# Performance work log

Hardware: AMD Instinct MI355X
Metric: run time of the kernel (lower is better)

The kernel has to match this reference:

```python
import jax, jax.numpy as jnp
import numpy as np

WS = 8      # window size
C = 64      # channels
B, H, W = 2, 256, 256
DMAX = 48   # max disparity


def setup_inputs() -> dict:
    key = jax.random.key(0)
    ks = jax.random.split(key, 16)
    n = lambda k, s, sc=1.0: jax.random.normal(k, s, dtype=jnp.float32) * sc
    return {
        'x_left': n(ks[0], (B, C, H, W)),
        'x_right': n(ks[1], (B, C, H, W)),
        'catfea_left': n(ks[2], (B, 4 * C, H, W)),
        'catfea_right': n(ks[3], (B, 4 * C, H, W)),
        'd_left': jax.random.randint(ks[4], (B, H, W), 0, DMAX, dtype=jnp.int32),
        'd_right': jax.random.randint(ks[5], (B, H, W), 0, DMAX, dtype=jnp.int32),
        # BatchNorm2d(4c) affine params (training-mode batch stats used in forward)
        'bn_gamma': jnp.ones((4 * C,), jnp.float32),
        'bn_beta': jnp.zeros((4 * C,), jnp.float32),
        # ResB: two grouped 3x3 convs, groups=4, 4c->4c  => weight [4c, c, 3, 3]
        'rb_w1': n(ks[6], (4 * C, C, 3, 3), 0.05), 'rb_b1': n(ks[7], (4 * C,), 0.05),
        'rb_w2': n(ks[8], (4 * C, C, 3, 3), 0.05), 'rb_b2': n(ks[9], (4 * C,), 0.05),
        # bq/bs: grouped 1x1 convs, groups=4, 4c->c => weight [c, c, 1, 1]
        'bq_w': n(ks[10], (C, C, 1, 1), 0.05), 'bq_b': n(ks[11], (C,), 0.05),
        'bs_w': n(ks[12], (C, C, 1, 1), 0.05), 'bs_b': n(ks[13], (C,), 0.05),
    }


def reference(x_left, x_right, catfea_left, catfea_right, d_left, d_right,
              bn_gamma, bn_beta, rb_w1, rb_b1, rb_w2, rb_b2,
              bq_w, bq_b, bs_w, bs_b):
    b, c, h, w = x_left.shape
    hn, wn = h // WS, w // WS
    P = WS * WS

    def conv(x, wgt, bias, pad):
        y = jax.lax.conv_general_dilated(
            x, wgt, (1, 1), [(pad, pad), (pad, pad)],
            dimension_numbers=('NCHW', 'OIHW', 'NCHW'), feature_group_count=4)
        return y + bias[None, :, None, None]

    def bn(x):
        mu = jnp.mean(x, axis=(0, 2, 3), keepdims=True)
        var = jnp.var(x, axis=(0, 2, 3), keepdims=True)
        return bn_gamma[None, :, None, None] * (x - mu) * jax.lax.rsqrt(var + 1e-5) + bn_beta[None, :, None, None]

    def resb(x):
        y = conv(x, rb_w1, rb_b1, 1)
        y = jnp.where(y > 0, y, 0.1 * y)  # LeakyReLU(0.1)
        y = conv(y, rb_w2, rb_b2, 1)
        return y + x

    # NOTE: faithfully replicates the original reshape-based patchify, which is
    # also applied to [b,h,w,c]-ordered gathered tensors (flat reinterpretation).
    def patchify(t):
        return t.reshape(b, c, hn, WS, wn, WS).transpose(0, 2, 4, 3, 5, 1)

    def unpatchify(t, ch):
        return t.reshape(b, hn, wn, WS, WS, ch).transpose(0, 5, 1, 3, 2, 4).reshape(b, ch, h, w)

    def gather_w(t, idx):  # t:[b,c,h,w], idx:[b,h,w] -> [b,h,w,c]
        return jnp.take_along_axis(t.transpose(0, 2, 3, 1), idx[..., None], axis=2)

    coords_w = jnp.arange(w, dtype=jnp.int32)[None, None, :]
    dl = d_left.astype(jnp.int32)
    dr = d_right.astype(jnp.int32)
    m_left = ((coords_w - dl) >= 0)[:, None].astype(x_left.dtype)
    m_right = ((coords_w + dr) <= w - 1)[:, None].astype(x_right.dtype)
    r2l_w = jnp.maximum(coords_w - dl, 0)
    l2r_w = jnp.minimum(coords_w + dr, w - 1)

    Q = conv(resb(bn(catfea_left)), bq_w, bq_b, 0)
    K = conv(resb(bn(catfea_right)), bs_w, bs_b, 0)

    Q_sel = patchify(gather_w(Q, l2r_w))
    K_sel = patchify(gather_w(K, r2l_w))
    Q_sel = Q_sel - Q_sel.mean((4, 5), keepdims=True)
    K_sel = K_sel - K_sel.mean((4, 5), keepdims=True)

    # per-window [P, c] @ [c, P] batched matmuls
    score_r2l = patchify(Q).reshape(-1, P, c) @ K_sel.transpose(0, 1, 2, 5, 3, 4).reshape(-1, c, P)
    score_l2r = patchify(K).reshape(-1, P, c) @ Q_sel.transpose(0, 1, 2, 5, 3, 4).reshape(-1, c, P)
    Mr2l = jax.nn.softmax(score_r2l, axis=-1)
    Ml2r = jax.nn.softmax(score_l2r, axis=-1)

    def m_relax(M, p=2):  # sum of row-shifted copies (shifts -p..p, zero-padded)
        out = M
        for s in range(1, p + 1):
            out = out + jnp.pad(M[:, :-s, :], ((0, 0), (s, 0), (0, 0)))
            out = out + jnp.pad(M[:, s:, :], ((0, 0), (0, s), (0, 0)))
        return out

    # Valid-mask maps (dead code w.r.t. returned outputs in the original; kept for fidelity)
    V_left = jnp.tanh(5 * unpatchify(jax.lax.stop_gradient(
        jnp.einsum('npq,nqp->np', m_relax(Mr2l), Ml2r)), 1))
    V_right = jnp.tanh(5 * unpatchify(jax.lax.stop_gradient(
        jnp.einsum('npq,nqp->np', m_relax(Ml2r), Mr2l)), 1))
    del V_left, V_right

    x_right_sel = patchify(gather_w(x_right, r2l_w)).reshape(-1, P, c)
    x_left_sel = patchify(gather_w(x_left, l2r_w)).reshape(-1, P, c)
    x_leftT = unpatchify(Mr2l @ x_right_sel, c)
    x_rightT = unpatchify(Ml2r @ x_left_sel, c)

    out_left = x_left + x_leftT * m_left
    out_right = x_right + x_rightT * m_right
    return out_left, out_right
```

## Files before the change

### kernel.cpp

```cpp
#include <hip/hip_runtime.h>


__global__ __launch_bounds__(256) void k_bnstats(
    const float* __restrict__ cat_l, const float* __restrict__ cat_r,
    const float* __restrict__ gamma, const float* __restrict__ beta,
    float* __restrict__ stats)
{
    int ch = blockIdx.x & 255;
    int side = blockIdx.x >> 8;
    const float* src = side ? cat_r : cat_l;
    int tid = threadIdx.x;
    float s = 0.f, s2 = 0.f;
    #pragma unroll
    for (int b = 0; b < 2; ++b) {
        const float* p = src + (size_t)b * 16777216 + (size_t)ch * 65536;
        for (int i = tid; i < 65536; i += 256) {
            float v = p[i];
            s += v; s2 += v * v;
        }
    }
    __shared__ float rs[256], rq[256];
    rs[tid] = s; rq[tid] = s2;
    __syncthreads();
    for (int off = 128; off > 0; off >>= 1) {
        if (tid < off) { rs[tid] += rs[tid + off]; rq[tid] += rq[tid + off]; }
        __syncthreads();
    }
    if (tid == 0) {
        float mean = rs[0] * (1.f / 131072.f);
        float var  = rq[0] * (1.f / 131072.f) - mean * mean;
        float rstd = rsqrtf(var + 1e-5f);
        float sc = gamma[ch] * rstd;
        stats[side * 512 + ch] = sc;
        stats[side * 512 + 256 + ch] = beta[ch] - mean * sc;
    }
}

__global__ __launch_bounds__(256) void k_fold(
    const float* __restrict__ w2, const float* __restrict__ b2,
    const float* __restrict__ bqw, const float* __restrict__ bqb,
    const float* __restrict__ bsw, const float* __restrict__ bsb,
    const float* __restrict__ stats,
    float* __restrict__ WfQ, float* __restrict__ bfQ,
    float* __restrict__ WfK, float* __restrict__ bfK)
{
    int idx = blockIdx.x * 256 + threadIdx.x;
    int j    = idx & 15;
    int ic   = (idx >> 4) & 63;
    int g    = (idx >> 10) & 3;
    int side = (idx >> 12) & 1;
    const float* pw  = side ? bsw : bqw;
    const float* st  = stats + side * 512;
    const float* pwr = pw + (size_t)(g * 16 + j) * 64;
    const float* wbase = w2 + (size_t)(g * 64) * 576 + ic * 9;
    float a[9] = {0.f,0.f,0.f,0.f,0.f,0.f,0.f,0.f,0.f};
    #pragma unroll 4
    for (int oc = 0; oc < 64; ++oc) {
        float p = pwr[oc];
        const float* wrow = wbase + (size_t)oc * 576;
        #pragma unroll
        for (int k = 0; k < 9; ++k) a[k] = fmaf(p, wrow[k], a[k]);
    }
    float* dst = (side ? WfK : WfQ) + (size_t)((g * 64 + ic) * 16 + j) * 12;
    #pragma unroll
    for (int k = 0; k < 9; ++k) dst[k] = a[k];
    dst[9]  = pwr[ic] * st[g * 64 + ic];
    dst[10] = 0.f; dst[11] = 0.f;
    if (ic == 0) {
        float s = (side ? bsb : bqb)[g * 16 + j];
        for (int oc = 0; oc < 64; ++oc)
            s = fmaf(pwr[oc], b2[g * 64 + oc] + st[256 + g * 64 + oc], s);
        (side ? bfK : bfQ)[g * 16 + j] = s;
    }
}

__global__ __launch_bounds__(256) void k_conv1(
    const float* __restrict__ cat, const float* __restrict__ stats,
    const float* __restrict__ w1, const float* __restrict__ b1,
    float* __restrict__ y1)
{
    int blk = blockIdx.x;
    int wt = blk & 7;   blk >>= 3;
    int ht = blk & 7;   blk >>= 3;
    int oh = blk & 3;   blk >>= 2;
    int g  = blk & 3;   blk >>= 2;
    int b  = blk;
    int tid = threadIdx.x;
    int tw = tid & 31, th = tid >> 5;
    int rb = th * 4;
    int h = ht * 32 + rb, w = wt * 32 + tw;

    __shared__ __align__(16) float tile[2][34][36];
    __shared__ __align__(16) float wb[2][16][12];

    float accA[16], accB[16], accC[16], accD[16];
    #pragma unroll
    for (int j = 0; j < 16; ++j) {
        float bb = b1[g * 64 + oh * 16 + j];
        accA[j] = bb; accB[j] = bb; accC[j] = bb; accD[j] = bb;
    }

    const float* catg = cat + ((size_t)b * 256 + g * 64) * 65536;
    const float* wg = w1 + (size_t)(g * 64 + oh * 16) * 576;
    int h0 = ht * 32 - 1, w0 = wt * 32 - 1;

    int soff[5]; int slds[5]; bool sin[5];
    #pragma unroll
    for (int s = 0; s < 5; ++s) {
        int idx = tid + 256 * s;
        int r = idx / 34, c = idx - r * 34;
        bool v = idx < 1156;
        int hh = h0 + r, ww = w0 + c;
        sin[s]  = v && (unsigned)hh < 256u && (unsigned)ww < 256u;
        soff[s] = hh * 256 + ww;
        slds[s] = v ? (r * 36 + c) : (33 * 36 + 35);
    }
    bool wvld = tid < 144;
    int woc = tid / 9, wk = tid - woc * 9;
    const float* wptr = wg + (size_t)woc * 576 + wk;
    int wlds = woc * 12 + wk;

    float t[5], wv, csn, shn;
    float* tile0 = &tile[0][0][0];
    float* wb0 = &wb[0][0][0];

    {
        csn = stats[g * 64]; shn = stats[256 + g * 64];
        #pragma unroll
        for (int s = 0; s < 5; ++s) {
            t[s] = sin[s] ? catg[soff[s]] : 0.f;
            tile0[slds[s]] = sin[s] ? fmaf(t[s], csn, shn) : 0.f;
        }
        if (wvld) wb0[wlds] = wptr[0];
    }
    __syncthreads();

    int cur = 0;
    for (int ic = 0; ic < 64; ++ic) {
        bool pf = (ic + 1 < 64);
        if (pf) {
            const float* plane = catg + (size_t)(ic + 1) * 65536;
            csn = stats[g * 64 + ic + 1];
            shn = stats[256 + g * 64 + ic + 1];
            #pragma unroll
            for (int s = 0; s < 5; ++s) t[s] = sin[s] ? plane[soff[s]] : 0.f;
            wv = wvld ? wptr[(ic + 1) * 9] : 0.f;
        }
        float xr[6][3];
        #pragma unroll
        for (int rr = 0; rr < 6; ++rr)
            #pragma unroll
            for (int cc = 0; cc < 3; ++cc)
                xr[rr][cc] = tile[cur][rb + rr][tw + cc];
        #pragma unroll
        for (int j = 0; j < 16; ++j) {
            float4 wa = *(const float4*)&wb[cur][j][0];
            float4 wc = *(const float4*)&wb[cur][j][4];
            float w8  = wb[cur][j][8];
            float s0 = accA[j], s1 = accB[j], s2 = accC[j], s3 = accD[j];
            s0 = fmaf(wa.x, xr[0][0], s0); s1 = fmaf(wa.x, xr[1][0], s1);
            s2 = fmaf(wa.x, xr[2][0], s2); s3 = fmaf(wa.x, xr[3][0], s3);
            s0 = fmaf(wa.y, xr[0][1], s0); s1 = fmaf(wa.y, xr[1][1], s1);
            s2 = fmaf(wa.y, xr[2][1], s2); s3 = fmaf(wa.y, xr[3][1], s3);
            s0 = fmaf(wa.z, xr[0][2], s0); s1 = fmaf(wa.z, xr[1][2], s1);
            s2 = fmaf(wa.z, xr[2][2], s2); s3 = fmaf(wa.z, xr[3][2], s3);
            s0 = fmaf(wa.w, xr[1][0], s0); s1 = fmaf(wa.w, xr[2][0], s1);
            s2 = fmaf(wa.w, xr[3][0], s2); s3 = fmaf(wa.w, xr[4][0], s3);
            s0 = fmaf(wc.x, xr[1][1], s0); s1 = fmaf(wc.x, xr[2][1], s1);
            s2 = fmaf(wc.x, xr[3][1], s2); s3 = fmaf(wc.x, xr[4][1], s3);
            s0 = fmaf(wc.y, xr[1][2], s0); s1 = fmaf(wc.y, xr[2][2], s1);
            s2 = fmaf(wc.y, xr[3][2], s2); s3 = fmaf(wc.y, xr[4][2], s3);
            s0 = fmaf(wc.z, xr[2][0], s0); s1 = fmaf(wc.z, xr[3][0], s1);
            s2 = fmaf(wc.z, xr[4][0], s2); s3 = fmaf(wc.z, xr[5][0], s3);
            s0 = fmaf(wc.w, xr[2][1], s0); s1 = fmaf(wc.w, xr[3][1], s1);
            s2 = fmaf(wc.w, xr[4][1], s2); s3 = fmaf(wc.w, xr[5][1], s3);
            s0 = fmaf(w8,   xr[2][2], s0); s1 = fmaf(w8,   xr[3][2], s1);
            s2 = fmaf(w8,   xr[4][2], s2); s3 = fmaf(w8,   xr[5][2], s3);
            accA[j] = s0; accB[j] = s1; accC[j] = s2; accD[j] = s3;
        }
        if (pf) {
            float* tn = &tile[cur ^ 1][0][0];
            #pragma unroll
            for (int s = 0; s < 5; ++s)
                tn[slds[s]] = sin[s] ? fmaf(t[s], csn, shn) : 0.f;
            if (wvld) (&wb[cur ^ 1][0][0])[wlds] = wv;
        }
        __syncthreads();
        cur ^= 1;
    }

    float* yp = y1 + ((size_t)b * 256 + g * 64 + oh * 16) * 65536
                   + (size_t)h * 256 + w;
    #pragma unroll
    for (int j = 0; j < 16; ++j) {
        float v0 = accA[j], v1 = accB[j], v2 = accC[j], v3 = accD[j];
        yp[(size_t)j * 65536 +   0] = v0 > 0.f ? v0 : 0.1f * v0;
        yp[(size_t)j * 65536 + 256] = v1 > 0.f ? v1 : 0.1f * v1;
        yp[(size_t)j * 65536 + 512] = v2 > 0.f ? v2 : 0.1f * v2;
        yp[(size_t)j * 65536 + 768] = v3 > 0.f ? v3 : 0.1f * v3;
    }
}

__global__ __launch_bounds__(256) void k_conv2f(
    const float* __restrict__ y1, const float* __restrict__ cat,
    const float* __restrict__ Wf, const float* __restrict__ bf,
    float* __restrict__ Qout)
{
    int blk = blockIdx.x;
    int wt = blk & 7;   blk >>= 3;
    int ht = blk & 7;   blk >>= 3;
    int g  = blk & 3;   blk >>= 2;
    int b  = blk;
    int tid = threadIdx.x;
    int tw = tid & 31, th = tid >> 5;
    int rb = th * 4;
    int h = ht * 32 + rb, w = wt * 32 + tw;

    __shared__ __align__(16) float tile[2][34][36];
    __shared__ __align__(16) float wb[2][16][12];

    float accA[16], accB[16], accC[16], accD[16];
    #pragma unroll
    for (int j = 0; j < 16; ++j) {
        float bb = bf[g * 16 + j];
        accA[j] = bb; accB[j] = bb; accC[j] = bb; accD[j] = bb;
    }

    const float* yg = y1 + ((size_t)b * 256 + g * 64) * 65536;
    const float* catp = cat + ((size_t)b * 256 + g * 64) * 65536
                            + (size_t)h * 256 + w;
    const float* wfg = Wf + (size_t)(g * 64) * 192;
    int h0 = ht * 32 - 1, w0 = wt * 32 - 1;

    int soff[5]; int slds[5]; bool sin[5];
    #pragma unroll
    for (int s = 0; s < 5; ++s) {
        int idx = tid + 256 * s;
        int r = idx / 34, c = idx - r * 34;
        bool v = idx < 1156;
        int hh = h0 + r, ww = w0 + c;
        sin[s]  = v && (unsigned)hh < 256u && (unsigned)ww < 256u;
        soff[s] = hh * 256 + ww;
        slds[s] = v ? (r * 36 + c) : (33 * 36 + 35);
    }
    bool wvld = tid < 192;
    float t[5], wv, cv0, cv1, cv2, cv3, ncv0, ncv1, ncv2, ncv3;
    float* tile0 = &tile[0][0][0];

    {
        #pragma unroll
        for (int s = 0; s < 5; ++s) {
            t[s] = sin[s] ? yg[soff[s]] : 0.f;
            tile0[slds[s]] = t[s];
        }
        if (wvld) (&wb[0][0][0])[tid] = wfg[tid];
        cv0 = catp[0]; cv1 = catp[256]; cv2 = catp[512]; cv3 = catp[768];
    }
    __syncthreads();

    int cur = 0;
    for (int ic = 0; ic < 64; ++ic) {
        bool pf = (ic + 1 < 64);
        if (pf) {
            const float* plane = yg + (size_t)(ic + 1) * 65536;
            #pragma unroll
            for (int s = 0; s < 5; ++s) t[s] = sin[s] ? plane[soff[s]] : 0.f;
            wv = wvld ? wfg[(size_t)(ic + 1) * 192 + tid] : 0.f;
            const float* cp = catp + (size_t)(ic + 1) * 65536;
            ncv0 = cp[0]; ncv1 = cp[256]; ncv2 = cp[512]; ncv3 = cp[768];
        }
        float xr[6][3];
        #pragma unroll
        for (int rr = 0; rr < 6; ++rr)
            #pragma unroll
            for (int cc = 0; cc < 3; ++cc)
                xr[rr][cc] = tile[cur][rb + rr][tw + cc];
        #pragma unroll
        for (int j = 0; j < 16; ++j) {
            float4 wa = *(const float4*)&wb[cur][j][0];
            float4 wc = *(const float4*)&wb[cur][j][4];
            float4 wd = *(const float4*)&wb[cur][j][8];
            float s0 = accA[j], s1 = accB[j], s2 = accC[j], s3 = accD[j];
            s0 = fmaf(wa.x, xr[0][0], s0); s1 = fmaf(wa.x, xr[1][0], s1);
            s2 = fmaf(wa.x, xr[2][0], s2); s3 = fmaf(wa.x, xr[3][0], s3);
            s0 = fmaf(wa.y, xr[0][1], s0); s1 = fmaf(wa.y, xr[1][1], s1);
            s2 = fmaf(wa.y, xr[2][1], s2); s3 = fmaf(wa.y, xr[3][1], s3);
            s0 = fmaf(wa.z, xr[0][2], s0); s1 = fmaf(wa.z, xr[1][2], s1);
            s2 = fmaf(wa.z, xr[2][2], s2); s3 = fmaf(wa.z, xr[3][2], s3);
            s0 = fmaf(wa.w, xr[1][0], s0); s1 = fmaf(wa.w, xr[2][0], s1);
            s2 = fmaf(wa.w, xr[3][0], s2); s3 = fmaf(wa.w, xr[4][0], s3);
            s0 = fmaf(wc.x, xr[1][1], s0); s1 = fmaf(wc.x, xr[2][1], s1);
            s2 = fmaf(wc.x, xr[3][1], s2); s3 = fmaf(wc.x, xr[4][1], s3);
            s0 = fmaf(wc.y, xr[1][2], s0); s1 = fmaf(wc.y, xr[2][2], s1);
            s2 = fmaf(wc.y, xr[3][2], s2); s3 = fmaf(wc.y, xr[4][2], s3);
            s0 = fmaf(wc.z, xr[2][0], s0); s1 = fmaf(wc.z, xr[3][0], s1);
            s2 = fmaf(wc.z, xr[4][0], s2); s3 = fmaf(wc.z, xr[5][0], s3);
            s0 = fmaf(wc.w, xr[2][1], s0); s1 = fmaf(wc.w, xr[3][1], s1);
            s2 = fmaf(wc.w, xr[4][1], s2); s3 = fmaf(wc.w, xr[5][1], s3);
            s0 = fmaf(wd.x, xr[2][2], s0); s1 = fmaf(wd.x, xr[3][2], s1);
            s2 = fmaf(wd.x, xr[4][2], s2); s3 = fmaf(wd.x, xr[5][2], s3);
            s0 = fmaf(wd.y, cv0, s0);      s1 = fmaf(wd.y, cv1, s1);
            s2 = fmaf(wd.y, cv2, s2);      s3 = fmaf(wd.y, cv3, s3);
            accA[j] = s0; accB[j] = s1; accC[j] = s2; accD[j] = s3;
        }
        if (pf) {
            float* tn = &tile[cur ^ 1][0][0];
            #pragma unroll
            for (int s = 0; s < 5; ++s) tn[slds[s]] = t[s];
            if (wvld) (&wb[cur ^ 1][0][0])[tid] = wv;
            cv0 = ncv0; cv1 = ncv1; cv2 = ncv2; cv3 = ncv3;
        }
        __syncthreads();
        cur ^= 1;
    }

    float* qp = Qout + ((size_t)b * 64 + g * 16) * 65536 + (size_t)h * 256 + w;
    #pragma unroll
    for (int j = 0; j < 16; ++j) {
        qp[(size_t)j * 65536 +   0] = accA[j];
        qp[(size_t)j * 65536 + 256] = accB[j];
        qp[(size_t)j * 65536 + 512] = accC[j];
        qp[(size_t)j * 65536 + 768] = accD[j];
    }
}

__global__ __launch_bounds__(256) void k_gather(
    const float* __restrict__ Kb, const float* __restrict__ Qb,
    const float* __restrict__ xr, const float* __restrict__ xl,
    const int* __restrict__ dl, const int* __restrict__ dr,
    float* __restrict__ GK, float* __restrict__ GQ,
    float* __restrict__ Gxr, float* __restrict__ Gxl)
{
    int blk = blockIdx.x;
    int h = blk & 255; blk >>= 8;
    int b = blk & 1;   blk >>= 1;
    int sel = blk;
    const float* src; float* dst; const int* dd; int r2l;
    if (sel == 0)      { src = Kb; dst = GK;  dd = dl; r2l = 1; }
    else if (sel == 1) { src = Qb; dst = GQ;  dd = dr; r2l = 0; }
    else if (sel == 2) { src = xr; dst = Gxr; dd = dl; r2l = 1; }
    else               { src = xl; dst = Gxl; dd = dr; r2l = 0; }
    const int* drow = dd + ((size_t)b * 256 + h) * 256;
    const float* sp = src + (size_t)b * 4194304 + h * 256;
    float* dp = dst + ((size_t)b * 256 + h) * 16384;
    int tid = threadIdx.x;
    for (int i = tid; i < 16384; i += 256) {
        int w = i >> 6, cc = i & 63;
        int d = drow[w];
        int wi = r2l ? (w - d < 0 ? 0 : w - d) : (w + d > 255 ? 255 : w + d);
        dp[i] = sp[(size_t)cc * 65536 + wi];
    }
}

__global__ __launch_bounds__(256) void k_attn(
    const float* __restrict__ Qb, const float* __restrict__ Kb,
    const float* __restrict__ GK, const float* __restrict__ GQ,
    const float* __restrict__ Gxr, const float* __restrict__ Gxl,
    const float* __restrict__ xl, const float* __restrict__ xr,
    const int* __restrict__ dl, const int* __restrict__ dr,
    float* __restrict__ out)
{
    int blk = blockIdx.x;
    int wn = blk & 31; blk >>= 5;
    int hn = blk & 31; blk >>= 5;
    int b  = blk & 1;  blk >>= 1;
    int dir = blk;

    const float* Amat = dir ? Kb : Qb;
    const float* Bg   = dir ? GQ : GK;
    const float* Xg   = dir ? Gxl : Gxr;
    const float* base = dir ? xr : xl;
    const int*  dd    = dir ? dr : dl;
    float* op = out + (size_t)dir * 8388608;

    __shared__ float A[64][65];
    __shared__ float Bm[64][65];
    __shared__ float S[64][65];
    __shared__ float rowsum[64];
    __shared__ float pmean[8];

    int tid = threadIdx.x;
    size_t abase = (size_t)b * 4194304 + (size_t)(hn * 8) * 256 + wn * 8;
    for (int i = tid; i < 4096; i += 256) {
        int cc = i >> 6, p1 = i & 63;
        A[p1][cc] = Amat[abase + (size_t)cc * 65536 + (p1 >> 3) * 256 + (p1 & 7)];
    }
    size_t gbase = (size_t)b * 4194304 + hn * 2048 + wn * 8;
    for (int i = tid; i < 4096; i += 256) {
        int cc = i >> 6, p2 = i & 63;
        Bm[p2][cc] = Bg[gbase + (size_t)cc * 65536 + (p2 >> 3) * 256 + (p2 & 7)];
    }
    __syncthreads();
    if (tid < 64) {
        float s = 0.f;
        #pragma unroll 8
        for (int cc = 0; cc < 64; ++cc) s += Bm[tid][cc];
        rowsum[tid] = s;
    }
    __syncthreads();
    if (tid < 8) {
        float s = 0.f;
        #pragma unroll
        for (int q = 0; q < 8; ++q) s += rowsum[tid * 8 + q];
        pmean[tid] = s * (1.f / 512.f);
    }
    __syncthreads();
    for (int i = tid; i < 4096; i += 256) {
        int p2 = i >> 6, cc = i & 63;
        Bm[p2][cc] -= pmean[p2 >> 3];
    }
    __syncthreads();

    int tp = (tid >> 4) << 2;
    int tc = (tid & 15) << 2;
    {
        float accs[4][4] = {};
        for (int cc = 0; cc < 64; ++cc) {
            float av[4], bv[4];
            #pragma unroll
            for (int i = 0; i < 4; ++i) av[i] = A[tp + i][cc];
            #pragma unroll
            for (int j = 0; j < 4; ++j) bv[j] = Bm[tc + j][cc];
            #pragma unroll
            for (int i = 0; i < 4; ++i)
                #pragma unroll
                for (int j = 0; j < 4; ++j)
                    accs[i][j] = fmaf(av[i], bv[j], accs[i][j]);
        }
        #pragma unroll
        for (int i = 0; i < 4; ++i)
            #pragma unroll
            for (int j = 0; j < 4; ++j)
                S[tp + i][tc + j] = accs[i][j];
    }
    __syncthreads();
    if (tid < 64) {
        float m = -3.0e38f;
        #pragma unroll 8
        for (int j = 0; j < 64; ++j) m = fmaxf(m, S[tid][j]);
        float ssum = 0.f;
        #pragma unroll 8
        for (int j = 0; j < 64; ++j) {
            float e = __expf(S[tid][j] - m);
            S[tid][j] = e; ssum += e;
        }
        float inv = 1.f / ssum;
        #pragma unroll 8
        for (int j = 0; j < 64; ++j) S[tid][j] *= inv;
    }
    __syncthreads();
    for (int i = tid; i < 4096; i += 256) {
        int cc = i >> 6, p2 = i & 63;
        Bm[p2][cc] = Xg[gbase + (size_t)cc * 65536 + (p2 >> 3) * 256 + (p2 & 7)];
    }
    __syncthreads();
    {
        float accs[4][4] = {};
        for (int p2 = 0; p2 < 64; ++p2) {
            float sv[4], xv[4];
            #pragma unroll
            for (int i = 0; i < 4; ++i) sv[i] = S[tp + i][p2];
            #pragma unroll
            for (int j = 0; j < 4; ++j) xv[j] = Bm[p2][tc + j];
            #pragma unroll
            for (int i = 0; i < 4; ++i)
                #pragma unroll
                for (int j = 0; j < 4; ++j)
                    accs[i][j] = fmaf(sv[i], xv[j], accs[i][j]);
        }
        #pragma unroll
        for (int i = 0; i < 4; ++i) {
            int p1 = tp + i;
            int h1 = hn * 8 + (p1 >> 3), w1 = wn * 8 + (p1 & 7);
            int d = dd[(size_t)b * 65536 + h1 * 256 + w1];
            float msk = dir ? ((w1 + d <= 255) ? 1.f : 0.f)
                            : ((w1 - d >= 0) ? 1.f : 0.f);
            #pragma unroll
            for (int j = 0; j < 4; ++j) {
                int ch = tc + j;
                size_t o = (size_t)b * 4194304 + (size_t)ch * 65536 + (size_t)h1 * 256 + w1;
                op[o] = fmaf(accs[i][j], msk, base[o]);
            }
        }
    }
}

extern "C" void kernel_launch(void* const* d_in, const int* in_sizes, int n_in,
                              void* d_out, int out_size, void* d_ws, size_t ws_size,
                              hipStream_t stream) {
    (void)in_sizes; (void)n_in; (void)out_size; (void)ws_size;
    const float* x_left  = (const float*)d_in[0];
    const float* x_right = (const float*)d_in[1];
    const float* cat_l   = (const float*)d_in[2];
    const float* cat_r   = (const float*)d_in[3];
    const int*   d_left  = (const int*)d_in[4];
    const int*   d_right = (const int*)d_in[5];
    const float* gamma   = (const float*)d_in[6];
    const float* beta    = (const float*)d_in[7];
    const float* rb_w1   = (const float*)d_in[8];
    const float* rb_b1   = (const float*)d_in[9];
    const float* rb_w2   = (const float*)d_in[10];
    const float* rb_b2   = (const float*)d_in[11];
    const float* bq_w    = (const float*)d_in[12];
    const float* bq_b    = (const float*)d_in[13];
    const float* bs_w    = (const float*)d_in[14];
    const float* bs_b    = (const float*)d_in[15];
    float* out = (float*)d_out;
    float* ws  = (float*)d_ws;

    float* y1    = ws;
    float* GK    = ws;
    float* GQ    = ws + 8388608;
    float* Gxr   = ws + 16777216;
    float* Gxl   = ws + 25165824;
    float* Qb    = ws + 33554432;
    float* Kb    = ws + 41943040;
    float* stats = ws + 50331648;
    float* WfQ = Kb;
    float* bfQ = Kb + 49152;
    float* WfK = out;
    float* bfK = out + 49152;

    k_bnstats<<<512, 256, 0, stream>>>(cat_l, cat_r, gamma, beta, stats);
    k_fold<<<32, 256, 0, stream>>>(rb_w2, rb_b2, bq_w, bq_b, bs_w, bs_b, stats,
                                   WfQ, bfQ, WfK, bfK);
    k_conv1<<<2048, 256, 0, stream>>>(cat_l, stats, rb_w1, rb_b1, y1);
    k_conv2f<<<512, 256, 0, stream>>>(y1, cat_l, WfQ, bfQ, Qb);
    k_conv1<<<2048, 256, 0, stream>>>(cat_r, stats + 512, rb_w1, rb_b1, y1);
    k_conv2f<<<512, 256, 0, stream>>>(y1, cat_r, WfK, bfK, Kb);
    k_gather<<<2048, 256, 0, stream>>>(Kb, Qb, x_right, x_left, d_left, d_right,
                                       GK, GQ, Gxr, Gxl);
    k_attn<<<4096, 256, 0, stream>>>(Qb, Kb, GK, GQ, Gxr, Gxl,
                                     x_left, x_right, d_left, d_right, out);
}
```

Before: 2.838 ms.

## Remap conv1 thread tiling to 4x4 pixel blocks per wavefront-owned channels

Result: faster. 2.366 ms (-16.6%).

```diff
diff --git a/kernel.cpp b/kernel.cpp
--- a/kernel.cpp
+++ b/kernel.cpp
@@ -86,18 +86,22 @@
     int g  = blk & 3;   blk >>= 2;
     int b  = blk;
     int tid = threadIdx.x;
-    int tw = tid & 31, th = tid >> 5;
-    int rb = th * 4;
-    int h = ht * 32 + rb, w = wt * 32 + tw;
+    int wid = tid >> 6;
+    int lane = tid & 63;
+    int rg = lane >> 3, cg = lane & 7;
+    int r4 = rg * 4, c4 = cg * 4;
 
     __shared__ __align__(16) float tile[2][34][36];
     __shared__ __align__(16) float wb[2][16][12];
 
     float accA[16], accB[16], accC[16], accD[16];
-    #pragma unroll
-    for (int j = 0; j < 16; ++j) {
-        float bb = b1[g * 64 + oh * 16 + j];
-        accA[j] = bb; accB[j] = bb; accC[j] = bb; accD[j] = bb;
+    {
+        int ob = g * 64 + oh * 16 + wid * 4;
+        float b0 = b1[ob], b1v = b1[ob + 1], b2v = b1[ob + 2], b3v = b1[ob + 3];
+        #pragma unroll
+        for (int p = 0; p < 16; ++p) {
+            accA[p] = b0; accB[p] = b1v; accC[p] = b2v; accD[p] = b3v;
+        }
     }
 
     const float* catg = cat + ((size_t)b * 256 + g * 64) * 65536;
@@ -146,38 +150,43 @@
             for (int s = 0; s < 5; ++s) t[s] = sin[s] ? plane[soff[s]] : 0.f;
             wv = wvld ? wptr[(ic + 1) * 9] : 0.f;
         }
-        float xr[6][3];
-        #pragma unroll
-        for (int rr = 0; rr < 6; ++rr)
-            #pragma unroll
-            for (int cc = 0; cc < 3; ++cc)
-                xr[rr][cc] = tile[cur][rb + rr][tw + cc];
-        #pragma unroll
-        for (int j = 0; j < 16; ++j) {
-            float4 wa = *(const float4*)&wb[cur][j][0];
-            float4 wc = *(const float4*)&wb[cur][j][4];
-            float w8  = wb[cur][j][8];
-            float s0 = accA[j], s1 = accB[j], s2 = accC[j], s3 = accD[j];
-            s0 = fmaf(wa.x, xr[0][0], s0); s1 = fmaf(wa.x, xr[1][0], s1);
-            s2 = fmaf(wa.x, xr[2][0], s2); s3 = fmaf(wa.x, xr[3][0], s3);
-            s0 = fmaf(wa.y, xr[0][1], s0); s1 = fmaf(wa.y, xr[1][1], s1);
-            s2 = fmaf(wa.y, xr[2][1], s2); s3 = fmaf(wa.y, xr[3][1], s3);
-            s0 = fmaf(wa.z, xr[0][2], s0); s1 = fmaf(wa.z, xr[1][2], s1);
-            s2 = fmaf(wa.z, xr[2][2], s2); s3 = fmaf(wa.z, xr[3][2], s3);
-            s0 = fmaf(wa.w, xr[1][0], s0); s1 = fmaf(wa.w, xr[2][0], s1);
-            s2 = fmaf(wa.w, xr[3][0], s2); s3 = fmaf(wa.w, xr[4][0], s3);
-            s0 = fmaf(wc.x, xr[1][1], s0); s1 = fmaf(wc.x, xr[2][1], s1);
-            s2 = fmaf(wc.x, xr[3][1], s2); s3 = fmaf(wc.x, xr[4][1], s3);
-            s0 = fmaf(wc.y, xr[1][2], s0); s1 = fmaf(wc.y, xr[2][2], s1);
-            s2 = fmaf(wc.y, xr[3][2], s2); s3 = fmaf(wc.y, xr[4][2], s3);
-            s0 = fmaf(wc.z, xr[2][0], s0); s1 = fmaf(wc.z, xr[3][0], s1);
-            s2 = fmaf(wc.z, xr[4][0], s2); s3 = fmaf(wc.z, xr[5][0], s3);
-            s0 = fmaf(wc.w, xr[2][1], s0); s1 = fmaf(wc.w, xr[3][1], s1);
-            s2 = fmaf(wc.w, xr[4][1], s2); s3 = fmaf(wc.w, xr[5][1], s3);
-            s0 = fmaf(w8,   xr[2][2], s0); s1 = fmaf(w8,   xr[3][2], s1);
-            s2 = fmaf(w8,   xr[4][2], s2); s3 = fmaf(w8,   xr[5][2], s3);
-            accA[j] = s0; accB[j] = s1; accC[j] = s2; accD[j] = s3;
-        }
+        float xr[6][6];
+        #pragma unroll
+        for (int r2 = 0; r2 < 6; ++r2) {
+            const float* rp = &tile[cur][r4 + r2][c4];
+            float4 v4 = *(const float4*)rp;
+            float2 v2 = *(const float2*)(rp + 4);
+            xr[r2][0] = v4.x; xr[r2][1] = v4.y; xr[r2][2] = v4.z;
+            xr[r2][3] = v4.w; xr[r2][4] = v2.x; xr[r2][5] = v2.y;
+        }
+        #define DO_OC(ACC, JO)                                              \
+        {                                                                   \
+            float4 wa = *(const float4*)&wb[cur][wid * 4 + JO][0];          \
+            float4 wc = *(const float4*)&wb[cur][wid * 4 + JO][4];          \
+            float w8  = wb[cur][wid * 4 + JO][8];                           \
+            _Pragma("unroll")                                               \
+            for (int rr = 0; rr < 4; ++rr) {                                \
+                _Pragma("unroll")                                           \
+                for (int cc = 0; cc < 4; ++cc) {                            \
+                    float s = ACC[rr * 4 + cc];                             \
+                    s = fmaf(wa.x, xr[rr    ][cc    ], s);                  \
+                    s = fmaf(wa.y, xr[rr    ][cc + 1], s);                  \
+                    s = fmaf(wa.z, xr[rr    ][cc + 2], s);                  \
+                    s = fmaf(wa.w, xr[rr + 1][cc    ], s);                  \
+                    s = fmaf(wc.x, xr[rr + 1][cc + 1], s);                  \
+                    s = fmaf(wc.y, xr[rr + 1][cc + 2], s);                  \
+                    s = fmaf(wc.z, xr[rr + 2][cc    ], s);                  \
+                    s = fmaf(wc.w, xr[rr + 2][cc + 1], s);                  \
+                    s = fmaf(w8,   xr[rr + 2][cc + 2], s);                  \
+                    ACC[rr * 4 + cc] = s;                                   \
+                }                                                           \
+            }                                                               \
+        }
+        DO_OC(accA, 0)
+        DO_OC(accB, 1)
+        DO_OC(accC, 2)
+        DO_OC(accD, 3)
+        #undef DO_OC
         if (pf) {
             float* tn = &tile[cur ^ 1][0][0];
             #pragma unroll
@@ -189,16 +198,28 @@
         cur ^= 1;
     }
 
-    float* yp = y1 + ((size_t)b * 256 + g * 64 + oh * 16) * 65536
-                   + (size_t)h * 256 + w;
-    #pragma unroll
-    for (int j = 0; j < 16; ++j) {
-        float v0 = accA[j], v1 = accB[j], v2 = accC[j], v3 = accD[j];
-        yp[(size_t)j * 65536 +   0] = v0 > 0.f ? v0 : 0.1f * v0;
-        yp[(size_t)j * 65536 + 256] = v1 > 0.f ? v1 : 0.1f * v1;
-        yp[(size_t)j * 65536 + 512] = v2 > 0.f ? v2 : 0.1f * v2;
-        yp[(size_t)j * 65536 + 768] = v3 > 0.f ? v3 : 0.1f * v3;
-    }
+    float* yp = y1 + ((size_t)b * 256 + g * 64 + oh * 16 + wid * 4) * 65536
+              + (size_t)(ht * 32 + r4) * 256 + wt * 32 + c4;
+    #define STORE_OC(ACC, JO)                                               \
+    {                                                                       \
+        float* op = yp + (size_t)(JO) * 65536;                              \
+        _Pragma("unroll")                                                   \
+        for (int rr = 0; rr < 4; ++rr) {                                    \
+            float v0 = ACC[rr * 4 + 0], v1 = ACC[rr * 4 + 1];               \
+            float v2 = ACC[rr * 4 + 2], v3 = ACC[rr * 4 + 3];               \
+            float4 o;                                                       \
+            o.x = v0 > 0.f ? v0 : 0.1f * v0;                                \
+            o.y = v1 > 0.f ? v1 : 0.1f * v1;                                \
+            o.z = v2 > 0.f ? v2 : 0.1f * v2;                                \
+            o.w = v3 > 0.f ? v3 : 0.1f * v3;                                \
+            *(float4*)(op + rr * 256) = o;                                  \
+        }                                                                   \
+    }
+    STORE_OC(accA, 0)
+    STORE_OC(accB, 1)
+    STORE_OC(accC, 2)
+    STORE_OC(accD, 3)
+    #undef STORE_OC
 }
 
 __global__ __launch_bounds__(256) void k_conv2f(
```
